# Kernel optimization log

Hardware: AMD Instinct MI355X
Metric: run time of the kernel (lower is better)

Reference implementation:

```python
import jax, jax.numpy as jnp
import numpy as np

DIM = 512
HEADS = 8
HEAD_DIM = DIM // HEADS
R = 2  # reduce_ratio
SCALE = HEAD_DIM ** -0.5


def setup_inputs() -> dict:
    key = jax.random.key(0)
    ks = jax.random.split(key, 8)
    bs, H, W = 4, 64, 64
    n = H * W
    std = 0.02
    x = jax.random.normal(ks[0], (bs, n, DIM), dtype=jnp.float32)
    q_w = jax.random.normal(ks[1], (DIM, DIM), dtype=jnp.float32) * std
    kv_w = jax.random.normal(ks[2], (DIM, 2 * DIM), dtype=jnp.float32) * std
    proj_w = jax.random.normal(ks[3], (DIM, DIM), dtype=jnp.float32) * std
    proj_b = jnp.zeros((DIM,), dtype=jnp.float32)
    # Conv2d(dim, dim, kernel=R, stride=R), kaiming-like init
    fan_out = R * R * DIM
    sr_w = jax.random.normal(ks[4], (DIM, DIM, R, R), dtype=jnp.float32) * np.sqrt(2.0 / fan_out)
    sr_b = jnp.zeros((DIM,), dtype=jnp.float32)
    ln_w = jnp.ones((DIM,), dtype=jnp.float32)
    ln_b = jnp.zeros((DIM,), dtype=jnp.float32)
    return {"x": x, "q_w": q_w, "kv_w": kv_w, "proj_w": proj_w, "proj_b": proj_b,
            "sr_w": sr_w, "sr_b": sr_b, "ln_w": ln_w, "ln_b": ln_b, "H": H, "W": W}


def _layernorm(x, w, b, eps=1e-5):
    mu = jnp.mean(x, axis=-1, keepdims=True)
    var = jnp.var(x, axis=-1, keepdims=True)
    return (x - mu) * jax.lax.rsqrt(var + eps) * w + b


def reference(x, q_w, kv_w, proj_w, proj_b, sr_w, sr_b, ln_w, ln_b, H, W):
    bs, n, ch = x.shape
    # q: (bs, heads, n, head_dim)
    q = (x @ q_w).reshape(bs, n, HEADS, HEAD_DIM).transpose(0, 2, 1, 3)
    # spatial reduction of kv source: strided conv + layernorm
    x_img = x.transpose(0, 2, 1).reshape(bs, ch, H, W)
    xr = jax.lax.conv_general_dilated(
        x_img, sr_w, window_strides=(R, R), padding='VALID',
        dimension_numbers=('NCHW', 'OIHW', 'NCHW')) + sr_b[None, :, None, None]
    xr = xr.reshape(bs, ch, -1).transpose(0, 2, 1)  # (bs, n_kv, ch)
    xr = _layernorm(xr, ln_w, ln_b)
    kv = xr @ kv_w  # (bs, n_kv, 2*ch)
    n_kv = kv.shape[1]
    kv = kv.reshape(bs, n_kv, 2, HEADS, HEAD_DIM).transpose(2, 0, 3, 1, 4)
    k, v = kv[0], kv[1]  # (bs, heads, n_kv, head_dim)
    att = jnp.einsum('bhqd,bhkd->bhqk', q, k) * SCALE
    att = jax.nn.softmax(att, axis=-1)
    net = jnp.einsum('bhqk,bhkd->bhqd', att, v)
    net = net.transpose(0, 2, 1, 3).reshape(bs, n, ch)
    return net @ proj_w + proj_b
```

## Files before the change

### kernel.cpp

```cpp
#include <hip/hip_runtime.h>
#include <cstdint>

#define HEADS 8
#define HD 64
#define NQ 4096
#define NKV 1024

typedef unsigned short u16;
typedef __attribute__((ext_vector_type(8))) short short8;
typedef __attribute__((ext_vector_type(4))) float f32x4;
typedef __attribute__((ext_vector_type(16))) float f32x16;

__device__ __forceinline__ u16 f2bf(float f){
  union { float f; unsigned u; } c; c.f = f;
  unsigned r = c.u + 0x7fffu + ((c.u >> 16) & 1u);
  return (u16)(r >> 16);
}
__device__ __forceinline__ unsigned pack2(float a, float b){
  return (unsigned)f2bf(a) | ((unsigned)f2bf(b) << 16);
}
__device__ __forceinline__ float fexp2(float x){
  float r;
  asm("v_exp_f32 %0, %1" : "=v"(r) : "v"(x));
  return r;
}
__device__ __forceinline__ unsigned cvtpk(float a, float b){
  unsigned r;
  asm("v_cvt_pk_bf16_f32 %0, %1, %2" : "=v"(r) : "v"(a), "v"(b));
  return r;
}
__device__ __forceinline__ void gll16(const void* g, void* l){
  __builtin_amdgcn_global_load_lds((const __attribute__((address_space(1))) unsigned*)g,
                                   (__attribute__((address_space(3))) unsigned*)l, 16, 0, 0);
}
#define SB0() __builtin_amdgcn_sched_barrier(0)
#define MFMA16(a, b, c) __builtin_amdgcn_mfma_f32_16x16x32_bf16(a, b, c, 0, 0, 0)
#define MFMA32(a, b, c) __builtin_amdgcn_mfma_f32_32x32x16_bf16(a, b, c, 0, 0, 0)
#define Z16 {0.f,0.f,0.f,0.f,0.f,0.f,0.f,0.f,0.f,0.f,0.f,0.f,0.f,0.f,0.f,0.f}

__global__ __launch_bounds__(256) void prep_all(const float* __restrict__ x,
                                                const float* __restrict__ q_w,
                                                const float* __restrict__ kv_w,
                                                const float* __restrict__ proj_w,
                                                const float* __restrict__ sr_w,
                                                u16* __restrict__ x_bf,
                                                u16* __restrict__ a_conv,
                                                u16* __restrict__ q_wT, u16* __restrict__ kv_wT,
                                                u16* __restrict__ proj_wT, u16* __restrict__ conv_BT){
  int bid = blockIdx.x;
  if (bid < 4096){
    int tid = bid * 256 + threadIdx.x;
    int b   = tid >> 18;
    int rem = tid & 262143;
    int pos = rem >> 6;
    int ci0 = (rem & 63) << 3;
    size_t src = ((size_t)(b * NQ + pos)) * 512 + ci0;
    const float4* s4 = (const float4*)(x + src);
    float4 v0 = s4[0], v1 = s4[1];
    uint4 p;
    p.x = pack2(v0.x, v0.y); p.y = pack2(v0.z, v0.w);
    p.z = pack2(v1.x, v1.y); p.w = pack2(v1.z, v1.w);
    *(uint4*)(x_bf + src) = p;
    int h = pos >> 6, w = pos & 63;
    int pr = (h >> 1) * 32 + (w >> 1);
    int t  = (h & 1) * 2 + (w & 1);
    *(uint4*)(a_conv + ((size_t)(b * NKV + pr)) * 2048 + t * 512 + ci0) = p;
    return;
  }
  int e = (bid - 4096) * 256 + threadIdx.x;
  if (e < 262144){ int n = e >> 9, k = e & 511; q_wT[e] = f2bf(q_w[k * 512 + n]); return; }
  e -= 262144;
  if (e < 524288){ int n = e >> 9, k = e & 511; kv_wT[e] = f2bf(kv_w[k * 1024 + n]); return; }
  e -= 524288;
  if (e < 262144){ int n = e >> 9, k = e & 511; proj_wT[e] = f2bf(proj_w[k * 512 + n]); return; }
  e -= 262144;
  { int co = e >> 11, r = e & 2047, t = r >> 9, ci = r & 511;
    conv_BT[e] = f2bf(sr_w[co * 2048 + ci * 4 + t]); }
}

__global__ __launch_bounds__(256) void gemm_qconv(const u16* __restrict__ x_bf, const u16* __restrict__ q_wT,
                                                  const u16* __restrict__ a_conv, const u16* __restrict__ conv_BT,
                                                  u16* __restrict__ q_sb, float* __restrict__ xr_pre,
                                                  float* __restrict__ xr_pre2, const float* __restrict__ sr_b){
  __shared__ __align__(16) u16 As[128 * 64];
  __shared__ __align__(16) u16 Bs[128 * 64];
  const int tid = threadIdx.x, lane = tid & 63, wave = tid >> 6;
  const int l15 = lane & 15, g = lane >> 4, r7 = l15 & 7;
  const int wr = wave >> 1, wc = wave & 1;
  int y = blockIdx.y;
  const u16 *A, *BT;
  int K, kb, m0, kz = 0;
  bool isQ;
  if (y < 128){ isQ = true;  A = x_bf;   BT = q_wT;    K = 512;  kb = 0;       m0 = y * 128; }
  else { y -= 128; kz = y >> 5;
         isQ = false; A = a_conv; BT = conv_BT; K = 2048; kb = kz << 9; m0 = (y & 31) * 128; }
  const int n0 = blockIdx.x * 128;
  f32x4 acc[4][4] = {};
  for (int i = 0; i < 8; ++i){
    int kt = kb + i * 64;
    #pragma unroll
    for (int ii = 0; ii < 4; ++ii){
      int c = ii * 256 + tid;
      int row = c >> 3, sc = (c & 7) ^ (row & 7);
      gll16(A  + (size_t)(m0 + row) * K + kt + sc * 8, As + (size_t)(ii * 256 + wave * 64) * 8);
      gll16(BT + (size_t)(n0 + row) * K + kt + sc * 8, Bs + (size_t)(ii * 256 + wave * 64) * 8);
    }
    __syncthreads();
    #pragma unroll
    for (int kk = 0; kk < 2; ++kk){
      short8 af[4];
      #pragma unroll
      for (int mi = 0; mi < 4; ++mi)
        af[mi] = *(const short8*)(As + (wr * 64 + mi * 16 + l15) * 64 + (((kk * 4 + g) ^ r7) << 3));
      #pragma unroll
      for (int ni = 0; ni < 4; ++ni){
        short8 bf = *(const short8*)(Bs + (wc * 64 + ni * 16 + l15) * 64 + (((kk * 4 + g) ^ r7) << 3));
        #pragma unroll
        for (int mi = 0; mi < 4; ++mi)
          acc[mi][ni] = MFMA16(af[mi], bf, acc[mi][ni]);
      }
    }
    __syncthreads();
  }
  #pragma unroll
  for (int mi = 0; mi < 4; ++mi){
    int row = m0 + wr * 64 + mi * 16 + (lane >> 4) * 4;
    #pragma unroll
    for (int ni = 0; ni < 4; ++ni){
      int col = n0 + wc * 64 + ni * 16 + l15;
      f32x4 v = acc[mi][ni];
      if (isQ){
        int h = col >> 6, d = col & 63;
        #pragma unroll
        for (int j = 0; j < 4; ++j){
          int r = row + j, b = r >> 12, nq = r & 4095;
          q_sb[(((size_t)(b * HEADS + h)) * NQ + nq) * HD + d] = f2bf(v[j] * 0.18033688f);
        }
      } else {
        float* Co = (kz < 2) ? (xr_pre + (size_t)kz * 4096 * 512)
                             : (xr_pre2 + (size_t)(kz - 2) * 4096 * 512);
        float bb = (kz == 0) ? sr_b[col] : 0.f;
        #pragma unroll
        for (int j = 0; j < 4; ++j) Co[(size_t)(row + j) * 512 + col] = v[j] + bb;
      }
    }
  }
}

template<int MODE>
__global__ __launch_bounds__(256) void gemm_bt(const u16* __restrict__ A, const u16* __restrict__ BT,
                                               float* __restrict__ Cf,
                                               u16* __restrict__ Cb0,
                                               u16* __restrict__ Cb1, const float* __restrict__ bias,
                                               int M, int N, int K){
  __shared__ __align__(16) u16 As[128 * 64];
  __shared__ __align__(16) u16 Bs[128 * 64];
  const int tid = threadIdx.x, lane = tid & 63, wave = tid >> 6;
  const int l15 = lane & 15, g = lane >> 4, r7 = l15 & 7;
  const int m0 = blockIdx.y * 128, n0 = blockIdx.x * 128;
  const int wr = wave >> 1, wc = wave & 1;
  f32x4 acc[4][4] = {};
  for (int kt = 0; kt < K; kt += 64){
    #pragma unroll
    for (int i = 0; i < 4; ++i){
      int c = i * 256 + tid;
      int row = c >> 3, sc = (c & 7) ^ (row & 7);
      gll16(A  + (size_t)(m0 + row) * K + kt + sc * 8, As + (size_t)(i * 256 + wave * 64) * 8);
      gll16(BT + (size_t)(n0 + row) * K + kt + sc * 8, Bs + (size_t)(i * 256 + wave * 64) * 8);
    }
    __syncthreads();
    #pragma unroll
    for (int kk = 0; kk < 2; ++kk){
      short8 af[4];
      #pragma unroll
      for (int mi = 0; mi < 4; ++mi)
        af[mi] = *(const short8*)(As + (wr * 64 + mi * 16 + l15) * 64 + (((kk * 4 + g) ^ r7) << 3));
      #pragma unroll
      for (int ni = 0; ni < 4; ++ni){
        short8 bf = *(const short8*)(Bs + (wc * 64 + ni * 16 + l15) * 64 + (((kk * 4 + g) ^ r7) << 3));
        #pragma unroll
        for (int mi = 0; mi < 4; ++mi)
          acc[mi][ni] = MFMA16(af[mi], bf, acc[mi][ni]);
      }
    }
    __syncthreads();
  }
  #pragma unroll
  for (int mi = 0; mi < 4; ++mi){
    int row = m0 + wr * 64 + mi * 16 + (lane >> 4) * 4;
    #pragma unroll
    for (int ni = 0; ni < 4; ++ni){
      int col = n0 + wc * 64 + ni * 16 + l15;
      f32x4 v = acc[mi][ni];
      if (MODE == 0){
        float bb = bias ? bias[col] : 0.f;
        #pragma unroll
        for (int j = 0; j < 4; ++j) Cf[(size_t)(row + j) * N + col] = v[j] + bb;
      } else {
        int s = col >> 9, h = (col >> 6) & 7, d = col & 63;
        if (s == 0){
          #pragma unroll
          for (int j = 0; j < 4; ++j){
            int r = row + j, b = r >> 10, p = r & 1023;
            Cb0[(((size_t)(b * HEADS + h)) * NKV + p) * HD + d] = f2bf(v[j]);
          }
        } else {
          int b = row >> 10, p0 = row & 1023;
          int pp = (p0 & ~12) | (((p0 >> 2) & 1) << 3) | (((p0 >> 3) & 1) << 2);
          ushort4 pk;
          pk.x = f2bf(v[0]); pk.y = f2bf(v[1]); pk.z = f2bf(v[2]); pk.w = f2bf(v[3]);
          *(ushort4*)(Cb1 + (((size_t)(b * HEADS + h)) * HD + d) * NKV + pp) = pk;
        }
      }
    }
  }
}

__global__ __launch_bounds__(256) void ln_k(const float* __restrict__ xp, const float* __restrict__ xp2,
                                            const float* __restrict__ w,
                                            const float* __restrict__ bias, u16* __restrict__ xr){
  int row = blockIdx.x * 4 + (threadIdx.x >> 6);
  int lane = threadIdx.x & 63;
  const float* s1 = xp  + (size_t)row * 512;
  const float* s2 = s1 + (size_t)4096 * 512;
  const float* s3 = xp2 + (size_t)row * 512;
  const float* s4 = s3 + (size_t)4096 * 512;
  float vals[8]; float s = 0.f, ss = 0.f;
  #pragma unroll
  for (int j = 0; j < 8; ++j){
    int c = lane + j * 64;
    float v = (s1[c] + s2[c]) + (s3[c] + s4[c]);
    vals[j] = v; s += v; ss += v * v;
  }
  #pragma unroll
  for (int off = 32; off >= 1; off >>= 1){ s += __shfl_xor(s, off); ss += __shfl_xor(ss, off); }
  float mean = s * (1.f / 512.f);
  float var  = ss * (1.f / 512.f) - mean * mean;
  float rs = rsqrtf(var + 1e-5f);
  u16* dst = xr + (size_t)row * 512;
  #pragma unroll
  for (int j = 0; j < 8; ++j){
    int c = lane + j * 64;
    dst[c] = f2bf((vals[j] - mean) * rs * w[c] + bias[c]);
  }
}

template<bool LAST>
__device__ __forceinline__ void attn_tile(const u16* ksb, const u16* vsb,
                                          u16* kstage, u16* vstage,
                                          const u16* akg, const u16* avg,
                                          const short8* qf,
                                          int l31, int hi, int x7,
                                          f32x16* o, float& l_run){
  asm volatile("s_waitcnt vmcnt(0)" ::: "memory");
  __builtin_amdgcn_s_barrier();
  SB0();

  f32x16 sa[2];
  __builtin_amdgcn_s_setprio(1);
  #pragma unroll
  for (int sub = 0; sub < 2; ++sub){
    f32x16 a = Z16;
    #pragma unroll
    for (int ks = 0; ks < 4; ++ks){
      short8 kf = *(const short8*)(ksb + (sub * 32 + l31) * 64 + (((ks * 2 + hi) ^ x7) << 3));
      a = MFMA32(kf, qf[ks], a);
    }
    sa[sub] = a;
  }
  __builtin_amdgcn_s_setprio(0);
  SB0();

  if (!LAST){
    gll16(akg,              kstage);
    gll16(akg + 2048,       kstage + 2048);
    gll16(avg,              vstage);
    gll16(avg + 32 * 1024,  vstage + 2048);
  }
  SB0();

  unsigned w[16];
  float ps = 0.f;
  #pragma unroll
  for (int sub = 0; sub < 2; ++sub)
    #pragma unroll
    for (int t = 0; t < 8; ++t){
      float p0 = fexp2(sa[sub][2 * t]), p1 = fexp2(sa[sub][2 * t + 1]);
      ps += p0 + p1;
      w[sub * 8 + t] = cvtpk(p0, p1);
    }
  l_run += ps;

  __builtin_amdgcn_s_setprio(1);
  #pragma unroll
  for (int dt = 0; dt < 2; ++dt)
    #pragma unroll
    for (int sl = 0; sl < 4; ++sl){
      short8 vf = *(const short8*)(vsb + (dt * 32 + l31) * 64 + (((sl * 2 + hi) ^ x7) << 3));
      union { unsigned u[4]; short8 s; } bb;
      bb.u[0] = w[sl * 4 + 0]; bb.u[1] = w[sl * 4 + 1];
      bb.u[2] = w[sl * 4 + 2]; bb.u[3] = w[sl * 4 + 3];
      o[dt] = MFMA32(vf, bb.s, o[dt]);
    }
  __builtin_amdgcn_s_setprio(0);
  SB0();
}

__global__ __launch_bounds__(256) void attn_k(const u16* __restrict__ q_s, const u16* __restrict__ k_s,
                                              const u16* __restrict__ vt_s, u16* __restrict__ net){
  __shared__ __align__(16) u16 Ks[2][64 * 64];
  __shared__ __align__(16) u16 Vt[2][64 * 64];
  const int tid = threadIdx.x, lane = tid & 63, wave = tid >> 6;
  const int l31 = lane & 31, hi = lane >> 5, x7 = lane & 7;
  const int id = blockIdx.x;
  const int xcd = id & 7, slot = id >> 3;
  const int bh = 4 * xcd + (slot >> 5);
  const int qblk = slot & 31;
  const u16* kb  = k_s  + (size_t)bh * NKV * HD;
  const u16* vtb = vt_s + (size_t)bh * HD * NKV;
  const int q0 = qblk * 128 + wave * 32;
  const u16* qbase = q_s + ((size_t)bh * NQ + q0 + l31) * HD + hi * 8;
  short8 qf[4];
  #pragma unroll
  for (int ks = 0; ks < 4; ++ks) qf[ks] = *(const short8*)(qbase + ks * 16);

  const int swz8 = (((tid & 7) ^ ((tid >> 3) & 7)) << 3);
  const u16* ak0 = kb  + (size_t)(tid >> 3) * 64   + swz8;
  const u16* av0 = vtb + (size_t)(tid >> 3) * 1024 + swz8;

  f32x16 o[2] = { Z16, Z16 };
  float l_run = 0.f;

  gll16(ak0,             &Ks[0][wave * 512]);
  gll16(ak0 + 2048,      &Ks[0][2048 + wave * 512]);
  gll16(av0,             &Vt[0][wave * 512]);
  gll16(av0 + 32 * 1024, &Vt[0][2048 + wave * 512]);

  for (int tt = 0; tt < 7; ++tt){
    attn_tile<false>(&Ks[0][0], &Vt[0][0], &Ks[1][wave * 512], &Vt[1][wave * 512],
                     ak0 + (size_t)(2 * tt + 1) * 4096, av0 + (2 * tt + 1) * 64,
                     qf, l31, hi, x7, o, l_run);
    attn_tile<false>(&Ks[1][0], &Vt[1][0], &Ks[0][wave * 512], &Vt[0][wave * 512],
                     ak0 + (size_t)(2 * tt + 2) * 4096, av0 + (2 * tt + 2) * 64,
                     qf, l31, hi, x7, o, l_run);
  }
  attn_tile<false>(&Ks[0][0], &Vt[0][0], &Ks[1][wave * 512], &Vt[1][wave * 512],
                   ak0 + (size_t)15 * 4096, av0 + 15 * 64,
                   qf, l31, hi, x7, o, l_run);
  attn_tile<true>(&Ks[1][0], &Vt[1][0], nullptr, nullptr, nullptr, nullptr,
                  qf, l31, hi, x7, o, l_run);

  float l = l_run + __shfl_xor(l_run, 32);
  float inv = 1.f / l;
  int b = bh >> 3, h = bh & 7;
  size_t obase = ((size_t)b * NQ + q0 + l31) * 512 + h * 64;
  #pragma unroll
  for (int dt = 0; dt < 2; ++dt)
    #pragma unroll
    for (int t = 0; t < 8; ++t){
      int j = 2 * t;
      int d = dt * 32 + (j & 3) + 8 * (j >> 2) + 4 * hi;
      *(unsigned*)(net + obase + d) = cvtpk(o[dt][j] * inv, o[dt][j + 1] * inv);
    }
}

extern "C" void kernel_launch(void* const* d_in, const int* in_sizes, int n_in,
                              void* d_out, int out_size, void* d_ws, size_t ws_size,
                              hipStream_t stream){
  const float* x      = (const float*)d_in[0];
  const float* q_w    = (const float*)d_in[1];
  const float* kv_w   = (const float*)d_in[2];
  const float* proj_w = (const float*)d_in[3];
  const float* proj_b = (const float*)d_in[4];
  const float* sr_w   = (const float*)d_in[5];
  const float* sr_b   = (const float*)d_in[6];
  const float* ln_w   = (const float*)d_in[7];
  const float* ln_b   = (const float*)d_in[8];
  (void)in_sizes; (void)n_in; (void)out_size; (void)ws_size;

  char* ws = (char*)d_ws;
  u16*   x_bf    = (u16*)(ws);
  float* xr_pre2 = (float*)(ws);
  u16*   a_conv  = (u16*)(ws + ((size_t)16 << 20));
  u16*   xr      = (u16*)(ws + ((size_t)16 << 20));
  u16*   net     = (u16*)(ws + ((size_t)16 << 20));
  u16*   q_sb    = (u16*)(ws + ((size_t)32 << 20));
  float* xr_pre  = (float*)(ws + ((size_t)48 << 20));
  u16*   k_sb    = (u16*)(ws + ((size_t)48 << 20));
  u16*   vt_sb   = (u16*)(ws + ((size_t)52 << 20));
  u16*   q_wT    = (u16*)(ws + ((size_t)64 << 20));
  u16*   kv_wT   = (u16*)(ws + ((size_t)64 << 20) + 524288);
  u16*   proj_wT = (u16*)(ws + ((size_t)64 << 20) + 524288 + 1048576);
  u16*   conv_BT = (u16*)(ws + ((size_t)64 << 20) + 524288 + 1048576 + 524288);
  float* out = (float*)d_out;

  prep_all<<<12288, 256, 0, stream>>>(x, q_w, kv_w, proj_w, sr_w,
                                      x_bf, a_conv, q_wT, kv_wT, proj_wT, conv_BT);
  gemm_qconv<<<dim3(4, 256), 256, 0, stream>>>(x_bf, q_wT, a_conv, conv_BT,
                                               q_sb, xr_pre, xr_pre2, sr_b);
  ln_k<<<1024, 256, 0, stream>>>(xr_pre, xr_pre2, ln_w, ln_b, xr);
  gemm_bt<2><<<dim3(8, 32),  256, 0, stream>>>(xr, kv_wT, nullptr, k_sb, vt_sb, nullptr, 4096, 1024, 512);
  attn_k<<<1024, 256, 0, stream>>>(q_sb, k_sb, vt_sb, net);
  gemm_bt<0><<<dim3(4, 128), 256, 0, stream>>>(net, proj_wT, out, nullptr, nullptr, proj_b, 16384, 512, 512);
}
```

Before: 143.3 us.

## Gather conv patches directly from x_bf and halve conv split-K partials

Removes the separate im2col a_conv buffer written in prep_all; the conv GEMM now computes patch addresses and loads straight from x_bf. The split-K for the strided conv drops from 4 slices to 2 (16 k-iterations each), so there are half as many fp32 partial buffers to write and for the layernorm kernel to read. The attention tile now issues the next K/V prefetch before the QK MFMAs. The trade-off is fewer conv blocks (less parallelism) and strided gathers in place of contiguous A loads.

```diff
diff --git a/kernel.cpp b/kernel.cpp
--- a/kernel.cpp
+++ b/kernel.cpp
@@ -44,27 +44,18 @@
                                                 const float* __restrict__ proj_w,
                                                 const float* __restrict__ sr_w,
                                                 u16* __restrict__ x_bf,
-                                                u16* __restrict__ a_conv,
                                                 u16* __restrict__ q_wT, u16* __restrict__ kv_wT,
                                                 u16* __restrict__ proj_wT, u16* __restrict__ conv_BT){
   int bid = blockIdx.x;
   if (bid < 4096){
     int tid = bid * 256 + threadIdx.x;
-    int b   = tid >> 18;
-    int rem = tid & 262143;
-    int pos = rem >> 6;
-    int ci0 = (rem & 63) << 3;
-    size_t src = ((size_t)(b * NQ + pos)) * 512 + ci0;
+    size_t src = (size_t)tid * 8;
     const float4* s4 = (const float4*)(x + src);
     float4 v0 = s4[0], v1 = s4[1];
     uint4 p;
     p.x = pack2(v0.x, v0.y); p.y = pack2(v0.z, v0.w);
     p.z = pack2(v1.x, v1.y); p.w = pack2(v1.z, v1.w);
     *(uint4*)(x_bf + src) = p;
-    int h = pos >> 6, w = pos & 63;
-    int pr = (h >> 1) * 32 + (w >> 1);
-    int t  = (h & 1) * 2 + (w & 1);
-    *(uint4*)(a_conv + ((size_t)(b * NKV + pr)) * 2048 + t * 512 + ci0) = p;
     return;
   }
   int e = (bid - 4096) * 256 + threadIdx.x;
@@ -79,31 +70,43 @@
 }
 
 __global__ __launch_bounds__(256) void gemm_qconv(const u16* __restrict__ x_bf, const u16* __restrict__ q_wT,
-                                                  const u16* __restrict__ a_conv, const u16* __restrict__ conv_BT,
+                                                  const u16* __restrict__ conv_BT,
                                                   u16* __restrict__ q_sb, float* __restrict__ xr_pre,
-                                                  float* __restrict__ xr_pre2, const float* __restrict__ sr_b){
+                                                  const float* __restrict__ sr_b){
   __shared__ __align__(16) u16 As[128 * 64];
   __shared__ __align__(16) u16 Bs[128 * 64];
   const int tid = threadIdx.x, lane = tid & 63, wave = tid >> 6;
   const int l15 = lane & 15, g = lane >> 4, r7 = l15 & 7;
   const int wr = wave >> 1, wc = wave & 1;
   int y = blockIdx.y;
-  const u16 *A, *BT;
-  int K, kb, m0, kz = 0;
-  bool isQ;
-  if (y < 128){ isQ = true;  A = x_bf;   BT = q_wT;    K = 512;  kb = 0;       m0 = y * 128; }
-  else { y -= 128; kz = y >> 5;
-         isQ = false; A = a_conv; BT = conv_BT; K = 2048; kb = kz << 9; m0 = (y & 31) * 128; }
+  const bool isQ = (y < 128);
+  int kz = 0, m0, kb = 0, iters, KB;
+  const u16* BT;
+  if (isQ){ m0 = y * 128; iters = 8;  KB = 512;  BT = q_wT; }
+  else { y -= 128; kz = y >> 5; m0 = (y & 31) * 128; kb = kz << 10; iters = 16; KB = 2048; BT = conv_BT; }
   const int n0 = blockIdx.x * 128;
+
+  unsigned aBase[4], bBase[4];
+  #pragma unroll
+  for (int ii = 0; ii < 4; ++ii){
+    int c = ii * 256 + tid;
+    int row = c >> 3, sc = (c & 7) ^ (row & 7);
+    if (isQ) aBase[ii] = (unsigned)(m0 + row) * 512 + sc * 8;
+    else { int grow = m0 + row, b = grow >> 10, pr = grow & 1023;
+           aBase[ii] = ((unsigned)(b * 4096) + (pr >> 5) * 128 + (pr & 31) * 2) * 512 + sc * 8; }
+    bBase[ii] = (unsigned)(n0 + row) * KB + sc * 8;
+  }
+
   f32x4 acc[4][4] = {};
-  for (int i = 0; i < 8; ++i){
+  for (int i = 0; i < iters; ++i){
     int kt = kb + i * 64;
+    unsigned aOff;
+    if (isQ) aOff = kt;
+    else { int t = kt >> 9; aOff = (unsigned)((t >> 1) * 64 + (t & 1)) * 512 + (kt & 511); }
     #pragma unroll
     for (int ii = 0; ii < 4; ++ii){
-      int c = ii * 256 + tid;
-      int row = c >> 3, sc = (c & 7) ^ (row & 7);
-      gll16(A  + (size_t)(m0 + row) * K + kt + sc * 8, As + (size_t)(ii * 256 + wave * 64) * 8);
-      gll16(BT + (size_t)(n0 + row) * K + kt + sc * 8, Bs + (size_t)(ii * 256 + wave * 64) * 8);
+      gll16(x_bf + aBase[ii] + aOff, As + (size_t)(ii * 256 + wave * 64) * 8);
+      gll16(BT + bBase[ii] + kt,     Bs + (size_t)(ii * 256 + wave * 64) * 8);
     }
     __syncthreads();
     #pragma unroll
@@ -137,8 +140,7 @@
           q_sb[(((size_t)(b * HEADS + h)) * NQ + nq) * HD + d] = f2bf(v[j] * 0.18033688f);
         }
       } else {
-        float* Co = (kz < 2) ? (xr_pre + (size_t)kz * 4096 * 512)
-                             : (xr_pre2 + (size_t)(kz - 2) * 4096 * 512);
+        float* Co = xr_pre + (size_t)kz * 4096 * 512;
         float bb = (kz == 0) ? sr_b[col] : 0.f;
         #pragma unroll
         for (int j = 0; j < 4; ++j) Co[(size_t)(row + j) * 512 + col] = v[j] + bb;
@@ -216,20 +218,18 @@
   }
 }
 
-__global__ __launch_bounds__(256) void ln_k(const float* __restrict__ xp, const float* __restrict__ xp2,
+__global__ __launch_bounds__(256) void ln_k(const float* __restrict__ xp,
                                             const float* __restrict__ w,
                                             const float* __restrict__ bias, u16* __restrict__ xr){
   int row = blockIdx.x * 4 + (threadIdx.x >> 6);
   int lane = threadIdx.x & 63;
-  const float* s1 = xp  + (size_t)row * 512;
+  const float* s1 = xp + (size_t)row * 512;
   const float* s2 = s1 + (size_t)4096 * 512;
-  const float* s3 = xp2 + (size_t)row * 512;
-  const float* s4 = s3 + (size_t)4096 * 512;
   float vals[8]; float s = 0.f, ss = 0.f;
   #pragma unroll
   for (int j = 0; j < 8; ++j){
     int c = lane + j * 64;
-    float v = (s1[c] + s2[c]) + (s3[c] + s4[c]);
+    float v = s1[c] + s2[c];
     vals[j] = v; s += v; ss += v * v;
   }
   #pragma unroll
@@ -256,21 +256,6 @@
   __builtin_amdgcn_s_barrier();
   SB0();
 
-  f32x16 sa[2];
-  __builtin_amdgcn_s_setprio(1);
-  #pragma unroll
-  for (int sub = 0; sub < 2; ++sub){
-    f32x16 a = Z16;
-    #pragma unroll
-    for (int ks = 0; ks < 4; ++ks){
-      short8 kf = *(const short8*)(ksb + (sub * 32 + l31) * 64 + (((ks * 2 + hi) ^ x7) << 3));
-      a = MFMA32(kf, qf[ks], a);
-    }
-    sa[sub] = a;
-  }
-  __builtin_amdgcn_s_setprio(0);
-  SB0();
-
   if (!LAST){
     gll16(akg,              kstage);
     gll16(akg + 2048,       kstage + 2048);
@@ -278,6 +263,20 @@
     gll16(avg + 32 * 1024,  vstage + 2048);
   }
   SB0();
+
+  f32x16 sa[2];
+  __builtin_amdgcn_s_setprio(1);
+  #pragma unroll
+  for (int sub = 0; sub < 2; ++sub){
+    f32x16 a = Z16;
+    #pragma unroll
+    for (int ks = 0; ks < 4; ++ks){
+      short8 kf = *(const short8*)(ksb + (sub * 32 + l31) * 64 + (((ks * 2 + hi) ^ x7) << 3));
+      a = MFMA32(kf, qf[ks], a);
+    }
+    sa[sub] = a;
+  }
+  __builtin_amdgcn_s_setprio(0);
 
   unsigned w[16];
   float ps = 0.f;
@@ -380,8 +379,6 @@
 
   char* ws = (char*)d_ws;
   u16*   x_bf    = (u16*)(ws);
-  float* xr_pre2 = (float*)(ws);
-  u16*   a_conv  = (u16*)(ws + ((size_t)16 << 20));
   u16*   xr      = (u16*)(ws + ((size_t)16 << 20));
   u16*   net     = (u16*)(ws + ((size_t)16 << 20));
   u16*   q_sb    = (u16*)(ws + ((size_t)32 << 20));
@@ -395,10 +392,9 @@
   float* out = (float*)d_out;
 
   prep_all<<<12288, 256, 0, stream>>>(x, q_w, kv_w, proj_w, sr_w,
-                                      x_bf, a_conv, q_wT, kv_wT, proj_wT, conv_BT);
-  gemm_qconv<<<dim3(4, 256), 256, 0, stream>>>(x_bf, q_wT, a_conv, conv_BT,
-                                               q_sb, xr_pre, xr_pre2, sr_b);
-  ln_k<<<1024, 256, 0, stream>>>(xr_pre, xr_pre2, ln_w, ln_b, xr);
+                                      x_bf, q_wT, kv_wT, proj_wT, conv_BT);
+  gemm_qconv<<<dim3(4, 192), 256, 0, stream>>>(x_bf, q_wT, conv_BT, q_sb, xr_pre, sr_b);
+  ln_k<<<1024, 256, 0, stream>>>(xr_pre, ln_w, ln_b, xr);
   gemm_bt<2><<<dim3(8, 32),  256, 0, stream>>>(xr, kv_wT, nullptr, k_sb, vt_sb, nullptr, 4096, 1024, 512);
   attn_k<<<1024, 256, 0, stream>>>(q_sb, k_sb, vt_sb, net);
   gemm_bt<0><<<dim3(4, 128), 256, 0, stream>>>(net, proj_wT, out, nullptr, nullptr, proj_b, 16384, 512, 512);
```

Result: faster. 140.4 us (-2.0%).
